# Kernel optimization log

Hardware: AMD Instinct MI355X
Metric: run time of the kernel (lower is better)

## Reference

```python
import jax, jax.numpy as jnp
import numpy as np

N_NODES = 50000
N_EDGES = 800000
IN_F = 128
HID = 256
N_CLS = 10
NUM_GRAPHS = 256


def setup_inputs() -> dict:
    key = jax.random.key(0)
    ks = jax.random.split(key, 8)
    x = jax.random.normal(ks[0], (N_NODES, IN_F), dtype=jnp.float32)
    edge_index = jax.random.randint(ks[1], (2, N_EDGES), 0, N_NODES, dtype=jnp.int64)
    batch = jnp.sort(jax.random.randint(ks[2], (N_NODES,), 0, NUM_GRAPHS, dtype=jnp.int64))
    # Glorot-style init for weights (GCNConv default), zeros bias
    W1 = jax.random.normal(ks[3], (IN_F, HID), dtype=jnp.float32) / np.sqrt(IN_F)
    b1 = jnp.zeros((HID,), dtype=jnp.float32)
    W2 = jax.random.normal(ks[4], (HID, HID), dtype=jnp.float32) / np.sqrt(HID)
    b2 = jnp.zeros((HID,), dtype=jnp.float32)
    Wlin = jax.random.normal(ks[5], (HID, N_CLS), dtype=jnp.float32) / np.sqrt(HID)
    blin = jnp.zeros((N_CLS,), dtype=jnp.float32)
    return {"x": x, "edge_index": edge_index, "batch": batch,
            "W1": W1, "b1": b1, "W2": W2, "b2": b2, "Wlin": Wlin, "blin": blin}


def reference(x, edge_index, batch, W1, b1, W2, b2, Wlin, blin):
    N = x.shape[0]
    # PyG GCNConv default: add self-loops, symmetric normalization D^-1/2 A D^-1/2
    loop = jnp.arange(N, dtype=edge_index.dtype)
    src = jnp.concatenate([edge_index[0], loop])  # message source (row)
    dst = jnp.concatenate([edge_index[1], loop])  # aggregation target (col)
    deg = jax.ops.segment_sum(jnp.ones_like(dst, dtype=x.dtype), dst, num_segments=N)
    dinv = jnp.where(deg > 0, jax.lax.rsqrt(deg), 0.0)
    norm = dinv[src] * dinv[dst]  # [E+N]

    def gcn_conv(h, W, b):
        h = h @ W                          # linear transform first (GCNConv)
        msg = h[src] * norm[:, None]       # gather + edge scale
        agg = jax.ops.segment_sum(msg, dst, num_segments=N)  # scatter-add
        return agg + b

    h = jax.nn.relu(gcn_conv(x, W1, b1))
    h = gcn_conv(h, W2, b2)

    # global_mean_pool over batch ids
    counts = jax.ops.segment_sum(jnp.ones((N,), x.dtype), batch, num_segments=NUM_GRAPHS)
    pooled = jax.ops.segment_sum(h, batch, num_segments=NUM_GRAPHS)
    pooled = pooled / jnp.maximum(counts, 1.0)[:, None]  # [NUM_GRAPHS, HID]

    return pooled @ Wlin + blin  # forward returns logits (softmax unused in forward)
```

## Files before the change

kernel.cpp:

```cpp
#include <hip/hip_runtime.h>
#include <hip/hip_bf16.h>

typedef __hip_bfloat16 bf16;
typedef __attribute__((ext_vector_type(8))) short short8;
typedef __attribute__((ext_vector_type(4))) float f32x4;
typedef __attribute__((ext_vector_type(2))) float f32x2;

#define N_NODES 50000
#define N_EDGES 800000
#define IN_F    128
#define HID     256
#define N_CLS   10
#define N_GRAPH 256

#define NB 98
#define PBLOCKS 256

__device__ __forceinline__ int IG(const int* __restrict__ p, int i, int w) {
    return w ? p[2 * i] : p[i];
}
__device__ __forceinline__ float LF(const void* __restrict__ p, int i, int isbf) {
    return isbf ? __bfloat162float(((const bf16*)p)[i]) : ((const float*)p)[i];
}
__device__ __forceinline__ float b2f(unsigned short h) {
    union { unsigned u; float f; } c; c.u = ((unsigned)h) << 16; return c.f;
}
__device__ __forceinline__ unsigned short f2b(float x) {
    bf16 h = __float2bfloat16(x);
    union { bf16 b; unsigned short u; } c; c.b = h; return c.u;
}
__device__ __forceinline__ float f8s(unsigned b) {
    union { unsigned u; float f; } c;
    c.u = ((b & 0x80u) << 24) | ((b & 0x7Fu) << 20);
    return c.f;
}
#define F8SCALE 0x1p120f
__device__ __forceinline__ unsigned f2fp8(float x) {
    unsigned short h = f2b(x * 0x1p-120f);
    unsigned s = ((unsigned)h >> 8) & 0x80u;
    unsigned mag = (unsigned)h & 0x7FFFu;
    unsigned r = (mag + 7u + ((mag >> 4) & 1u)) >> 4;
    if (r > 0x7Eu) r = 0x7Eu;
    return s | r;
}

#if defined(__has_builtin)
#if __has_builtin(__builtin_amdgcn_cvt_pk_f32_fp8)
#define HW_FP8 1
#endif
#if __has_builtin(__builtin_amdgcn_cvt_pk_fp8_f32)
#define HW_FP8E 1
#endif
#endif

__device__ __forceinline__ f32x2 cvt2lo(unsigned v) {
#ifdef HW_FP8
    return __builtin_amdgcn_cvt_pk_f32_fp8((int)v, false);
#else
    f32x2 r; r[0] = f8s(v & 0xFF) * F8SCALE; r[1] = f8s((v >> 8) & 0xFF) * F8SCALE; return r;
#endif
}
__device__ __forceinline__ f32x2 cvt2hi(unsigned v) {
#ifdef HW_FP8
    return __builtin_amdgcn_cvt_pk_f32_fp8((int)v, true);
#else
    f32x2 r; r[0] = f8s((v >> 16) & 0xFF) * F8SCALE; r[1] = f8s(v >> 24) * F8SCALE; return r;
#endif
}
__device__ __forceinline__ unsigned pk4_fp8(float v0, float v1, float v2, float v3) {
#ifdef HW_FP8E
    int o = __builtin_amdgcn_cvt_pk_fp8_f32(v0, v1, 0, false);
    o = __builtin_amdgcn_cvt_pk_fp8_f32(v2, v3, o, true);
    return (unsigned)o;
#else
    return f2fp8(v0) | (f2fp8(v1) << 8) | (f2fp8(v2) << 16) | (f2fp8(v3) << 24);
#endif
}

__global__ __launch_bounds__(256) void k_detect(const int* __restrict__ ei,
                                                const unsigned short* __restrict__ x,
                                                int* __restrict__ flags) {
    __shared__ int nz, cnt;
    if (threadIdx.x == 0) { nz = 0; cnt = 0; }
    __syncthreads();
    int found = 0, c = 0;
    for (int s = 0; s < 4; ++s) {
        int idx = 2 * (threadIdx.x * 4 + s) + 1;
        if (ei[idx] != 0) found = 1;
    }
    for (int s = 0; s < 8; ++s) {
        unsigned short h = x[threadIdx.x * 8 + s];
        int e = (h >> 7) & 0xFF;
        if (e >= 110 && e <= 135) c++;
    }
    if (found) atomicAdd(&nz, 1);
    atomicAdd(&cnt, c);
    __syncthreads();
    if (threadIdx.x == 0) {
        flags[0] = (nz == 0) ? 1 : 0;
        flags[1] = (cnt > 1536) ? 1 : 0;
    }
}

__global__ __launch_bounds__(256) void k_partA1(const int* __restrict__ ei, int* __restrict__ bucketCnt,
                                                int* __restrict__ blockBase, const int* __restrict__ flags,
                                                int E, int N) {
    __shared__ int h[NB];
    int t = threadIdx.x;
    if (t < NB) h[t] = 0;
    __syncthreads();
    int w = flags[0];
    for (int e = blockIdx.x * 256 + t; e < E; e += PBLOCKS * 256) {
        int d = IG(ei, E + e, w);
        int s = IG(ei, e, w);
        if ((unsigned)d < (unsigned)N && (unsigned)s < (unsigned)N)
            atomicAdd(&h[d >> 9], 1);
    }
    __syncthreads();
    if (t < NB)
        blockBase[blockIdx.x * NB + t] = atomicAdd(&bucketCnt[t * 16], h[t]);
}

__global__ __launch_bounds__(128) void k_bscan(const int* __restrict__ bucketCnt,
                                               int* __restrict__ bucketBase) {
    __shared__ int s[128];
    int t = threadIdx.x;
    int v = (t < NB) ? bucketCnt[t * 16] : 0;
    s[t] = v;
    __syncthreads();
    for (int off = 1; off < 128; off <<= 1) {
        int add = (t >= off) ? s[t - off] : 0;
        __syncthreads();
        s[t] += add;
        __syncthreads();
    }
    if (t <= NB) bucketBase[t] = (t < NB) ? (s[t] - v) : s[NB - 1] + 0;
    if (t == NB - 1) bucketBase[NB] = s[t];
}

__global__ __launch_bounds__(256) void k_partA2(const int* __restrict__ ei,
                                                const int* __restrict__ bucketBase,
                                                const int* __restrict__ blockBase,
                                                unsigned* __restrict__ part,
                                                const int* __restrict__ flags, int E, int N) {
    __shared__ int cur[NB];
    int t = threadIdx.x;
    if (t < NB) cur[t] = bucketBase[t] + blockBase[blockIdx.x * NB + t];
    __syncthreads();
    int w = flags[0];
    for (int e = blockIdx.x * 256 + t; e < E; e += PBLOCKS * 256) {
        int d = IG(ei, E + e, w);
        int s = IG(ei, e, w);
        if ((unsigned)d < (unsigned)N && (unsigned)s < (unsigned)N) {
            int slot = atomicAdd(&cur[d >> 9], 1);
            part[slot] = ((unsigned)(d & 511) << 16) | (unsigned)s;
        }
    }
}

__global__ __launch_bounds__(256) void k_partB(const unsigned* __restrict__ part,
                                               const int* __restrict__ bucketBase,
                                               int* __restrict__ rowptr, float* __restrict__ dinv,
                                               int* __restrict__ col, int N) {
    __shared__ int hist[512];
    __shared__ int scn[512];
    __shared__ int pair[256];
    int b = blockIdx.x, t = threadIdx.x;
    int s0 = bucketBase[b], e0 = bucketBase[b + 1];
    hist[t] = 0; hist[t + 256] = 0;
    __syncthreads();
    for (int j = s0 + t; j < e0; j += 256)
        atomicAdd(&hist[part[j] >> 16], 1);
    __syncthreads();
    int a0 = hist[2 * t], a1 = hist[2 * t + 1];
    int pv = a0 + a1;
    pair[t] = pv;
    __syncthreads();
    for (int off = 1; off < 256; off <<= 1) {
        int add = (t >= off) ? pair[t - off] : 0;
        __syncthreads();
        pair[t] += add;
        __syncthreads();
    }
    int pbase = pair[t] - pv;
    scn[2 * t] = pbase;
    scn[2 * t + 1] = pbase + a0;
    __syncthreads();
#pragma unroll
    for (int hh = 0; hh < 2; ++hh) {
        int l = t + hh * 256;
        int node = b * 512 + l;
        if (node < N) {
            rowptr[node] = s0 + scn[l];
            dinv[node] = rsqrtf((float)(hist[l] + 1));
        }
    }
    if (b == 0 && t == 0) rowptr[N] = bucketBase[NB];
    __syncthreads();
    for (int j = s0 + t; j < e0; j += 256) {
        unsigned p = part[j];
        int pos = s0 + atomicAdd(&scn[p >> 16], 1);
        col[pos] = (int)(p & 0xFFFFu);
    }
}

#define CVTX_BLOCKS 6250
#define CVT1_BLOCKS 128
#define CVT2_BLOCKS 256
#define GB_BLOCKS   196
__global__ __launch_bounds__(256) void k_cvt(const void* __restrict__ x, const float* __restrict__ dinv,
                                             unsigned char* __restrict__ xs8,
                                             const void* __restrict__ W1, unsigned short* __restrict__ w1t,
                                             const void* __restrict__ W2, unsigned short* __restrict__ w2t,
                                             const int* __restrict__ batch, int* __restrict__ gstart,
                                             const int* __restrict__ flags) {
    int b = blockIdx.x;
    int fb = flags[1];
    if (b < CVTX_BLOCKS) {
        int gid = b * 256 + threadIdx.x;
        int row = gid >> 5;
        float d = dinv[row];
        float vx, vy, vz, vw;
        if (fb) {
            ushort4 v = ((const ushort4*)x)[gid];
            vx = b2f(v.x); vy = b2f(v.y); vz = b2f(v.z); vw = b2f(v.w);
        } else {
            float4 v = ((const float4*)x)[gid];
            vx = v.x; vy = v.y; vz = v.z; vw = v.w;
        }
        ((unsigned*)xs8)[gid] = pk4_fp8(vx * d, vy * d, vz * d, vw * d);
    } else if (b < CVTX_BLOCKS + CVT1_BLOCKS) {
        int i = (b - CVTX_BLOCKS) * 256 + threadIdx.x;
        int n = i >> 7, k = i & 127;
        w1t[i] = f2b(LF(W1, k * 256 + n, fb));
    } else if (b < CVTX_BLOCKS + CVT1_BLOCKS + CVT2_BLOCKS) {
        int i = (b - CVTX_BLOCKS - CVT1_BLOCKS) * 256 + threadIdx.x;
        int n = i >> 8, k = i & 255;
        w2t[i] = f2b(LF(W2, k * 256 + n, fb));
    } else {
        int i = (b - CVTX_BLOCKS - CVT1_BLOCKS - CVT2_BLOCKS) * 256 + threadIdx.x;
        if (i <= N_NODES) {
            int w = flags[0];
            int prev = (i == 0) ? -1 : IG(batch, i - 1, w);
            int cur  = (i == N_NODES) ? N_GRAPH : IG(batch, i, w);
            if (prev < -1) prev = -1;
            if (cur > N_GRAPH) cur = N_GRAPH;
            for (int g = prev + 1; g <= cur; ++g)
                if (g >= 0 && g <= N_GRAPH) gstart[g] = i;
        }
    }
}

#define BSTR 132
__global__ __launch_bounds__(256) void k_gemm(const unsigned short* __restrict__ A,
                                              const unsigned short* __restrict__ Bt,
                                              unsigned short* __restrict__ C,
                                              unsigned char* __restrict__ C8, int M, int K,
                                              const float* __restrict__ rowscale,
                                              const void* __restrict__ bias,
                                              const int* __restrict__ flags, int relu) {
    __shared__ unsigned short Bs[128 * BSTR];
    int t = threadIdx.x;
    int lane = t & 63;
    int w = t >> 6;
    int stripe = blockIdx.y;
    int bm = blockIdx.x * 128;
    int l15 = lane & 15, quad = lane >> 4;
    const short8 Z8 = {0, 0, 0, 0, 0, 0, 0, 0};
    f32x4 acc[2][8];
#pragma unroll
    for (int i = 0; i < 2; ++i)
#pragma unroll
        for (int j = 0; j < 8; ++j) acc[i][j] = (f32x4){0.f, 0.f, 0.f, 0.f};

    int row0 = bm + w * 32 + l15;
    int row1 = row0 + 16;
    for (int kp = 0; kp < K; kp += 128) {
        if (kp) __syncthreads();
        {
            int n = t >> 1, h = t & 1;
            const unsigned short* src = &Bt[(size_t)(stripe * 128 + n) * K + kp + h * 64];
            unsigned short* dst = &Bs[n * BSTR + h * 64];
#pragma unroll
            for (int j = 0; j < 8; ++j)
                *(uint4*)&dst[j * 8] = *(const uint4*)&src[j * 8];
        }
        __syncthreads();
#pragma unroll
        for (int ks = 0; ks < 4; ++ks) {
            const unsigned short* abase = &A[(size_t)row0 * K + kp + ks * 32 + quad * 8];
            short8 a0 = (row0 < M) ? *(const short8*)abase : Z8;
            short8 a1 = (row1 < M) ? *(const short8*)(abase + (size_t)16 * K) : Z8;
#pragma unroll
            for (int tt = 0; tt < 8; ++tt) {
                short8 b = *(const short8*)&Bs[(tt * 16 + l15) * BSTR + ks * 32 + quad * 8];
                acc[0][tt] = __builtin_amdgcn_mfma_f32_16x16x32_bf16(b, a0, acc[0][tt], 0, 0, 0);
                acc[1][tt] = __builtin_amdgcn_mfma_f32_16x16x32_bf16(b, a1, acc[1][tt], 0, 0, 0);
            }
        }
    }
    int fb = flags[1];
    int rowA[2];
    float drow[2];
#pragma unroll
    for (int sa = 0; sa < 2; ++sa) {
        rowA[sa] = bm + w * 32 + sa * 16 + l15;
        drow[sa] = (rowscale && rowA[sa] < M) ? rowscale[rowA[sa]] : 1.f;
    }
    __syncthreads();
    if (C8) {
        unsigned* Cs = (unsigned*)Bs;
#pragma unroll
        for (int tt = 0; tt < 8; ++tt) {
            int colb = stripe * 128 + tt * 16 + quad * 4;
            float bc[4];
#pragma unroll
            for (int rr = 0; rr < 4; ++rr)
                bc[rr] = bias ? LF(bias, colb + rr, fb) : 0.f;
#pragma unroll
            for (int sa = 0; sa < 2; ++sa) {
                float v[4];
#pragma unroll
                for (int rr = 0; rr < 4; ++rr) {
                    float u = fmaf(acc[sa][tt][rr], drow[sa], bc[rr]);
                    v[rr] = relu ? fmaxf(u, 0.f) : u;
                }
                Cs[(w * 32 + sa * 16 + l15) * 36 + tt * 4 + quad] =
                    pk4_fp8(v[0], v[1], v[2], v[3]);
            }
        }
        __syncthreads();
        int r = t >> 1, h = t & 1;
        int grow = bm + r;
        if (grow < M) {
            const uint4* src = (const uint4*)(Cs + r * 36 + h * 16);
            uint4* dst = (uint4*)&C8[(size_t)grow * 256 + stripe * 128 + h * 64];
#pragma unroll
            for (int j = 0; j < 4; ++j) dst[j] = src[j];
        }
    } else {
        unsigned short* Cs = Bs;
#pragma unroll
        for (int tt = 0; tt < 8; ++tt) {
            int colb = stripe * 128 + tt * 16 + quad * 4;
            float bc[4];
#pragma unroll
            for (int rr = 0; rr < 4; ++rr)
                bc[rr] = bias ? LF(bias, colb + rr, fb) : 0.f;
#pragma unroll
            for (int sa = 0; sa < 2; ++sa) {
                float v[4];
#pragma unroll
                for (int rr = 0; rr < 4; ++rr) {
                    float u = fmaf(acc[sa][tt][rr], drow[sa], bc[rr]);
                    v[rr] = relu ? fmaxf(u, 0.f) : u;
                }
                ushort4 o;
                o.x = f2b(v[0]); o.y = f2b(v[1]); o.z = f2b(v[2]); o.w = f2b(v[3]);
                *(ushort4*)&Cs[(w * 32 + sa * 16 + l15) * 132 + tt * 16 + quad * 4] = o;
            }
        }
        __syncthreads();
        int r = t >> 1, h = t & 1;
        int grow = bm + r;
        if (grow < M) {
            int base = r * 132 + h * 64;
            size_t gbase = (size_t)grow * 256 + stripe * 128 + h * 64;
#pragma unroll
            for (int j = 0; j < 8; ++j) {
                uint2 a2 = *(const uint2*)&Cs[base + j * 8];
                uint2 b2 = *(const uint2*)&Cs[base + j * 8 + 4];
                uint4 u; u.x = a2.x; u.y = a2.y; u.z = b2.x; u.w = b2.y;
                *(uint4*)&C[gbase + j * 8] = u;
            }
        }
    }
}

__global__ __launch_bounds__(256) void k_agg2(const unsigned char* __restrict__ XS,
                                              const int* __restrict__ rowptr, const int* __restrict__ col,
                                              unsigned short* __restrict__ Hout, int N) {
    int lane = threadIdx.x & 63;
    int i = (blockIdx.x * 256 + threadIdx.x) >> 6;
    if (i >= N) return;
    int fo = lane * 2;
    unsigned sv = *(const unsigned short*)&XS[(size_t)i * 128 + fo];
    f32x2 a = cvt2lo(sv);
    int s = rowptr[i], e = rowptr[i + 1];
    int j = s;
    while (j + 16 <= e) {
        unsigned v[16];
#pragma unroll
        for (int q = 0; q < 16; ++q)
            v[q] = *(const unsigned short*)&XS[(size_t)col[j + q] * 128 + fo];
#pragma unroll
        for (int q = 0; q < 16; ++q) a += cvt2lo(v[q]);
        j += 16;
    }
    if (j + 8 <= e) {
        unsigned v[8];
#pragma unroll
        for (int q = 0; q < 8; ++q)
            v[q] = *(const unsigned short*)&XS[(size_t)col[j + q] * 128 + fo];
#pragma unroll
        for (int q = 0; q < 8; ++q) a += cvt2lo(v[q]);
        j += 8;
    }
    if (j + 4 <= e) {
        unsigned v[4];
#pragma unroll
        for (int q = 0; q < 4; ++q)
            v[q] = *(const unsigned short*)&XS[(size_t)col[j + q] * 128 + fo];
#pragma unroll
        for (int q = 0; q < 4; ++q) a += cvt2lo(v[q]);
        j += 4;
    }
    for (; j < e; ++j)
        a += cvt2lo(*(const unsigned short*)&XS[(size_t)col[j] * 128 + fo]);
    ushort2 o;
    o.x = f2b(a[0]); o.y = f2b(a[1]);
    *(ushort2*)&Hout[(size_t)i * 128 + fo] = o;
}

__global__ __launch_bounds__(256) void k_agg4(const unsigned char* __restrict__ XW,
                                              const int* __restrict__ rowptr, const int* __restrict__ col,
                                              const float* __restrict__ dinv, const void* __restrict__ bias,
                                              const int* __restrict__ flags,
                                              unsigned short* __restrict__ Hout, int N) {
    int lane = threadIdx.x & 63;
    int i = (blockIdx.x * 256 + threadIdx.x) >> 6;
    if (i >= N) return;
    int fo = lane * 4;
    unsigned sv = *(const unsigned*)&XW[(size_t)i * 256 + fo];
    f32x2 a01 = cvt2lo(sv), a23 = cvt2hi(sv);
    int s = rowptr[i], e = rowptr[i + 1];
    int j = s;
    while (j + 16 <= e) {
        unsigned v[16];
#pragma unroll
        for (int q = 0; q < 16; ++q)
            v[q] = *(const unsigned*)&XW[(size_t)col[j + q] * 256 + fo];
#pragma unroll
        for (int q = 0; q < 16; ++q) { a01 += cvt2lo(v[q]); a23 += cvt2hi(v[q]); }
        j += 16;
    }
    if (j + 8 <= e) {
        unsigned v[8];
#pragma unroll
        for (int q = 0; q < 8; ++q)
            v[q] = *(const unsigned*)&XW[(size_t)col[j + q] * 256 + fo];
#pragma unroll
        for (int q = 0; q < 8; ++q) { a01 += cvt2lo(v[q]); a23 += cvt2hi(v[q]); }
        j += 8;
    }
    if (j + 4 <= e) {
        unsigned v[4];
#pragma unroll
        for (int q = 0; q < 4; ++q)
            v[q] = *(const unsigned*)&XW[(size_t)col[j + q] * 256 + fo];
#pragma unroll
        for (int q = 0; q < 4; ++q) { a01 += cvt2lo(v[q]); a23 += cvt2hi(v[q]); }
        j += 4;
    }
    for (; j < e; ++j) {
        unsigned v = *(const unsigned*)&XW[(size_t)col[j] * 256 + fo];
        a01 += cvt2lo(v); a23 += cvt2hi(v);
    }
    int fb = flags[1];
    float di = dinv[i];
    float bx = LF(bias, fo + 0, fb), by = LF(bias, fo + 1, fb);
    float bz = LF(bias, fo + 2, fb), bw = LF(bias, fo + 3, fb);
    ushort4 o;
    o.x = f2b(fmaf(a01[0], di, bx)); o.y = f2b(fmaf(a01[1], di, by));
    o.z = f2b(fmaf(a23[0], di, bz)); o.w = f2b(fmaf(a23[1], di, bw));
    *(ushort4*)&Hout[(size_t)i * 256 + fo] = o;
}

__global__ __launch_bounds__(256) void k_poolfinal(const unsigned short* __restrict__ H2,
                                                   const int* __restrict__ gstart,
                                                   const void* __restrict__ Wlin,
                                                   const void* __restrict__ blin,
                                                   const int* __restrict__ flags,
                                                   void* __restrict__ outv) {
    __shared__ float red[4][256];
    __shared__ float p[256];
    int g = blockIdx.x, t = threadIdx.x;
    int sub = t >> 6, lane = t & 63;
    int s = gstart[g], e = gstart[g + 1];
    int cnt = e - s;
    float ax = 0.f, ay = 0.f, az = 0.f, aw = 0.f;
    for (int i = s + sub; i < e; i += 4) {
        ushort4 v = *(const ushort4*)&H2[(size_t)i * 256 + lane * 4];
        ax += b2f(v.x); ay += b2f(v.y); az += b2f(v.z); aw += b2f(v.w);
    }
    red[sub][lane * 4 + 0] = ax;
    red[sub][lane * 4 + 1] = ay;
    red[sub][lane * 4 + 2] = az;
    red[sub][lane * 4 + 3] = aw;
    __syncthreads();
    float inv = 1.f / fmaxf((float)cnt, 1.f);
    p[t] = (red[0][t] + red[1][t] + red[2][t] + red[3][t]) * inv;
    __syncthreads();
    int fb = flags[1];
    if (t < N_CLS) {
        float sum = LF(blin, t, fb);
        for (int f = 0; f < HID; ++f) sum = fmaf(p[f], LF(Wlin, f * N_CLS + t, fb), sum);
        if (fb) ((bf16*)outv)[g * N_CLS + t] = __float2bfloat16(sum);
        else    ((float*)outv)[g * N_CLS + t] = sum;
    }
}

extern "C" void kernel_launch(void* const* d_in, const int* in_sizes, int n_in,
                              void* d_out, int out_size, void* d_ws, size_t ws_size,
                              hipStream_t stream) {
    (void)n_in; (void)ws_size; (void)in_sizes; (void)out_size;
    const void* x     = d_in[0];
    const int*  ei    = (const int*)d_in[1];
    const int*  batch = (const int*)d_in[2];
    const void* W1    = d_in[3];
    const void* b1    = d_in[4];
    const void* W2    = d_in[5];
    const void* b2    = d_in[6];
    const void* Wl    = d_in[7];
    const void* bl    = d_in[8];

    const int N = N_NODES, E = N_EDGES, F = IN_F, H = HID, G = N_GRAPH;

    char* ws = (char*)d_ws;
    size_t off = 0;
    auto alloc = [&](size_t bytes) -> void* {
        void* p = ws + off;
        off += (bytes + 511) & ~(size_t)511;
        return p;
    };
    unsigned char*  xs8  = (unsigned char*)alloc((size_t)N * F);
    unsigned short* aggX = (unsigned short*)alloc((size_t)N * F * 2);
    unsigned short* H1   = (unsigned short*)alloc((size_t)N * H * 2);
    unsigned short* H2   = (unsigned short*)alloc((size_t)N * H * 2);
    unsigned char*  XW2s8 = xs8;
    unsigned short* w1t  = (unsigned short*)alloc((size_t)H * F * 2);
    unsigned short* w2t  = (unsigned short*)alloc((size_t)H * H * 2);
    int*   bucketCnt = (int*)alloc((size_t)NB * 16 * 4);
    int*   bucketBase = (int*)alloc((size_t)(NB + 1) * 4);
    int*   blockBase = (int*)alloc((size_t)PBLOCKS * NB * 4);
    unsigned* part  = (unsigned*)alloc((size_t)E * 4);
    int*   gstart  = (int*)alloc((size_t)(G + 1) * 4);
    float* dinv    = (float*)alloc((size_t)N * 4);
    int*   rowptr  = (int*)alloc((size_t)(N + 1) * 4);
    int*   flags   = (int*)alloc(512);
    int*   col     = (int*)alloc((size_t)E * 4);
    size_t zero_bytes = (size_t)NB * 16 * 4;

    hipMemsetAsync(bucketCnt, 0, zero_bytes, stream);

    k_detect<<<1, 256, 0, stream>>>(ei, (const unsigned short*)x, flags);
    k_partA1<<<PBLOCKS, 256, 0, stream>>>(ei, bucketCnt, blockBase, flags, E, N);
    k_bscan<<<1, 128, 0, stream>>>(bucketCnt, bucketBase);
    k_partA2<<<PBLOCKS, 256, 0, stream>>>(ei, bucketBase, blockBase, part, flags, E, N);
    k_partB<<<NB, 256, 0, stream>>>(part, bucketBase, rowptr, dinv, col, N);

    k_cvt<<<CVTX_BLOCKS + CVT1_BLOCKS + CVT2_BLOCKS + GB_BLOCKS, 256, 0, stream>>>(
        x, dinv, xs8, W1, w1t, W2, w2t, batch, gstart, flags);

    dim3 gemmGrid((N + 127) / 128, 2);
    int nbAgg = (N + 3) / 4;

    k_agg2<<<nbAgg, 256, 0, stream>>>(xs8, rowptr, col, aggX, N);
    k_gemm<<<gemmGrid, 256, 0, stream>>>(aggX, w1t, H1, nullptr, N, F, dinv, b1, flags, 1);
    k_gemm<<<gemmGrid, 256, 0, stream>>>(H1, w2t, nullptr, XW2s8, N, H, dinv, nullptr, flags, 0);
    k_agg4<<<nbAgg, 256, 0, stream>>>(XW2s8, rowptr, col, dinv, b2, flags, H2, N);
    k_poolfinal<<<G, 256, 0, stream>>>(H2, gstart, Wl, bl, flags, d_out);
}
```

Baseline: 282.8 us.

## Restructure GEMM to full-width 64-row tiles with register-prefetched direct global operands

The GEMM kernel no longer stages the B (weight) stripe in shared memory. Each block now covers 64 rows and all 256 output columns, and each wave owns a 64-column slice. A and B fragments are loaded straight from global memory into registers, with a one-step software prefetch of the next K slice. This removes the shared-memory staging and barriers and the second column-stripe grid dimension, so each A row is read once instead of twice. The cost is higher register pressure and B fragments reloaded from global/L2 by every block, with no LDS reuse.

```diff
diff --git a/kernel.cpp b/kernel.cpp
--- a/kernel.cpp
+++ b/kernel.cpp
@@ -251,7 +251,6 @@
     }
 }
 
-#define BSTR 132
 __global__ __launch_bounds__(256) void k_gemm(const unsigned short* __restrict__ A,
                                               const unsigned short* __restrict__ Bt,
                                               unsigned short* __restrict__ C,
@@ -259,120 +258,122 @@
                                               const float* __restrict__ rowscale,
                                               const void* __restrict__ bias,
                                               const int* __restrict__ flags, int relu) {
-    __shared__ unsigned short Bs[128 * BSTR];
+    __shared__ unsigned char lds[64 * 132 * 4];
     int t = threadIdx.x;
     int lane = t & 63;
     int w = t >> 6;
-    int stripe = blockIdx.y;
-    int bm = blockIdx.x * 128;
+    int bm = blockIdx.x * 64;
     int l15 = lane & 15, quad = lane >> 4;
-    const short8 Z8 = {0, 0, 0, 0, 0, 0, 0, 0};
-    f32x4 acc[2][8];
-#pragma unroll
-    for (int i = 0; i < 2; ++i)
-#pragma unroll
-        for (int j = 0; j < 8; ++j) acc[i][j] = (f32x4){0.f, 0.f, 0.f, 0.f};
-
-    int row0 = bm + w * 32 + l15;
-    int row1 = row0 + 16;
-    for (int kp = 0; kp < K; kp += 128) {
-        if (kp) __syncthreads();
-        {
-            int n = t >> 1, h = t & 1;
-            const unsigned short* src = &Bt[(size_t)(stripe * 128 + n) * K + kp + h * 64];
-            unsigned short* dst = &Bs[n * BSTR + h * 64];
-#pragma unroll
-            for (int j = 0; j < 8; ++j)
-                *(uint4*)&dst[j * 8] = *(const uint4*)&src[j * 8];
-        }
-        __syncthreads();
-#pragma unroll
-        for (int ks = 0; ks < 4; ++ks) {
-            const unsigned short* abase = &A[(size_t)row0 * K + kp + ks * 32 + quad * 8];
-            short8 a0 = (row0 < M) ? *(const short8*)abase : Z8;
-            short8 a1 = (row1 < M) ? *(const short8*)(abase + (size_t)16 * K) : Z8;
-#pragma unroll
-            for (int tt = 0; tt < 8; ++tt) {
-                short8 b = *(const short8*)&Bs[(tt * 16 + l15) * BSTR + ks * 32 + quad * 8];
-                acc[0][tt] = __builtin_amdgcn_mfma_f32_16x16x32_bf16(b, a0, acc[0][tt], 0, 0, 0);
-                acc[1][tt] = __builtin_amdgcn_mfma_f32_16x16x32_bf16(b, a1, acc[1][tt], 0, 0, 0);
-            }
-        }
-    }
+
+    f32x4 acc[4][4];
+#pragma unroll
+    for (int ar = 0; ar < 4; ++ar)
+#pragma unroll
+        for (int tt = 0; tt < 4; ++tt) acc[ar][tt] = (f32x4){0.f, 0.f, 0.f, 0.f};
+
+    const unsigned short* ap[4];
+    const unsigned short* bp[4];
+#pragma unroll
+    for (int ar = 0; ar < 4; ++ar)
+        ap[ar] = &A[(size_t)(bm + ar * 16 + l15) * K + quad * 8];
+#pragma unroll
+    for (int tt = 0; tt < 4; ++tt)
+        bp[tt] = &Bt[(size_t)(w * 64 + tt * 16 + l15) * K + quad * 8];
+
+    int nks = K >> 5;
+    short8 a[4], b[4];
+#pragma unroll
+    for (int ar = 0; ar < 4; ++ar) a[ar] = *(const short8*)(ap[ar]);
+#pragma unroll
+    for (int tt = 0; tt < 4; ++tt) b[tt] = *(const short8*)(bp[tt]);
+    for (int ks = 0; ks < nks; ++ks) {
+        short8 an[4], bn[4];
+        int nxt = (ks + 1) * 32;
+        if (ks + 1 < nks) {
+#pragma unroll
+            for (int ar = 0; ar < 4; ++ar) an[ar] = *(const short8*)(ap[ar] + nxt);
+#pragma unroll
+            for (int tt = 0; tt < 4; ++tt) bn[tt] = *(const short8*)(bp[tt] + nxt);
+        }
+#pragma unroll
+        for (int ar = 0; ar < 4; ++ar)
+#pragma unroll
+            for (int tt = 0; tt < 4; ++tt)
+                acc[ar][tt] = __builtin_amdgcn_mfma_f32_16x16x32_bf16(b[tt], a[ar], acc[ar][tt], 0, 0, 0);
+        if (ks + 1 < nks) {
+#pragma unroll
+            for (int ar = 0; ar < 4; ++ar) a[ar] = an[ar];
+#pragma unroll
+            for (int tt = 0; tt < 4; ++tt) b[tt] = bn[tt];
+        }
+    }
+
     int fb = flags[1];
-    int rowA[2];
-    float drow[2];
-#pragma unroll
-    for (int sa = 0; sa < 2; ++sa) {
-        rowA[sa] = bm + w * 32 + sa * 16 + l15;
-        drow[sa] = (rowscale && rowA[sa] < M) ? rowscale[rowA[sa]] : 1.f;
-    }
-    __syncthreads();
+    float drow[4];
+#pragma unroll
+    for (int ar = 0; ar < 4; ++ar) {
+        int row = bm + ar * 16 + l15;
+        drow[ar] = (rowscale && row < M) ? rowscale[row] : 1.f;
+    }
     if (C8) {
-        unsigned* Cs = (unsigned*)Bs;
-#pragma unroll
-        for (int tt = 0; tt < 8; ++tt) {
-            int colb = stripe * 128 + tt * 16 + quad * 4;
+        unsigned* Cs = (unsigned*)lds;
+#pragma unroll
+        for (int tt = 0; tt < 4; ++tt) {
+            int colb = w * 64 + tt * 16 + quad * 4;
             float bc[4];
 #pragma unroll
             for (int rr = 0; rr < 4; ++rr)
                 bc[rr] = bias ? LF(bias, colb + rr, fb) : 0.f;
 #pragma unroll
-            for (int sa = 0; sa < 2; ++sa) {
+            for (int ar = 0; ar < 4; ++ar) {
                 float v[4];
 #pragma unroll
                 for (int rr = 0; rr < 4; ++rr) {
-                    float u = fmaf(acc[sa][tt][rr], drow[sa], bc[rr]);
+                    float u = fmaf(acc[ar][tt][rr], drow[ar], bc[rr]);
                     v[rr] = relu ? fmaxf(u, 0.f) : u;
                 }
-                Cs[(w * 32 + sa * 16 + l15) * 36 + tt * 4 + quad] =
+                Cs[(ar * 16 + l15) * 68 + w * 16 + tt * 4 + quad] =
                     pk4_fp8(v[0], v[1], v[2], v[3]);
             }
         }
         __syncthreads();
-        int r = t >> 1, h = t & 1;
-        int grow = bm + r;
-        if (grow < M) {
-            const uint4* src = (const uint4*)(Cs + r * 36 + h * 16);
-            uint4* dst = (uint4*)&C8[(size_t)grow * 256 + stripe * 128 + h * 64];
-#pragma unroll
-            for (int j = 0; j < 4; ++j) dst[j] = src[j];
+        int r = t >> 2, h = t & 3;
+        if (bm + r < M) {
+            const unsigned* src = Cs + r * 68 + h * 16;
+            uint4* dst = (uint4*)&C8[(size_t)(bm + r) * 256 + h * 64];
+#pragma unroll
+            for (int j = 0; j < 4; ++j) dst[j] = *(const uint4*)(src + j * 4);
         }
     } else {
-        unsigned short* Cs = Bs;
-#pragma unroll
-        for (int tt = 0; tt < 8; ++tt) {
-            int colb = stripe * 128 + tt * 16 + quad * 4;
+        unsigned short* Cs = (unsigned short*)lds;
+#pragma unroll
+        for (int tt = 0; tt < 4; ++tt) {
+            int colb = w * 64 + tt * 16 + quad * 4;
             float bc[4];
 #pragma unroll
             for (int rr = 0; rr < 4; ++rr)
                 bc[rr] = bias ? LF(bias, colb + rr, fb) : 0.f;
 #pragma unroll
-            for (int sa = 0; sa < 2; ++sa) {
+            for (int ar = 0; ar < 4; ++ar) {
                 float v[4];
 #pragma unroll
                 for (int rr = 0; rr < 4; ++rr) {
-                    float u = fmaf(acc[sa][tt][rr], drow[sa], bc[rr]);
+                    float u = fmaf(acc[ar][tt][rr], drow[ar], bc[rr]);
                     v[rr] = relu ? fmaxf(u, 0.f) : u;
                 }
                 ushort4 o;
                 o.x = f2b(v[0]); o.y = f2b(v[1]); o.z = f2b(v[2]); o.w = f2b(v[3]);
-                *(ushort4*)&Cs[(w * 32 + sa * 16 + l15) * 132 + tt * 16 + quad * 4] = o;
+                *(ushort4*)&Cs[(ar * 16 + l15) * 264 + w * 64 + tt * 16 + quad * 4] = o;
             }
         }
         __syncthreads();
-        int r = t >> 1, h = t & 1;
-        int grow = bm + r;
-        if (grow < M) {
-            int base = r * 132 + h * 64;
-            size_t gbase = (size_t)grow * 256 + stripe * 128 + h * 64;
-#pragma unroll
-            for (int j = 0; j < 8; ++j) {
-                uint2 a2 = *(const uint2*)&Cs[base + j * 8];
-                uint2 b2 = *(const uint2*)&Cs[base + j * 8 + 4];
-                uint4 u; u.x = a2.x; u.y = a2.y; u.z = b2.x; u.w = b2.y;
-                *(uint4*)&C[gbase + j * 8] = u;
-            }
+        int r = t >> 2, h = t & 3;
+        if (bm + r < M) {
+            int base = r * 264 + h * 64;
+            size_t g = (size_t)(bm + r) * 256 + h * 64;
+#pragma unroll
+            for (int j = 0; j < 8; ++j)
+                *(uint4*)&C[g + j * 8] = *(const uint4*)&Cs[base + j * 8];
         }
     }
 }
@@ -562,12 +563,12 @@
     k_cvt<<<CVTX_BLOCKS + CVT1_BLOCKS + CVT2_BLOCKS + GB_BLOCKS, 256, 0, stream>>>(
         x, dinv, xs8, W1, w1t, W2, w2t, batch, gstart, flags);
 
-    dim3 gemmGrid((N + 127) / 128, 2);
+    int gemmBlocks = (N + 63) / 64;
     int nbAgg = (N + 3) / 4;
 
     k_agg2<<<nbAgg, 256, 0, stream>>>(xs8, rowptr, col, aggX, N);
-    k_gemm<<<gemmGrid, 256, 0, stream>>>(aggX, w1t, H1, nullptr, N, F, dinv, b1, flags, 1);
-    k_gemm<<<gemmGrid, 256, 0, stream>>>(H1, w2t, nullptr, XW2s8, N, H, dinv, nullptr, flags, 0);
+    k_gemm<<<gemmBlocks, 256, 0, stream>>>(aggX, w1t, H1, nullptr, N, F, dinv, b1, flags, 1);
+    k_gemm<<<gemmBlocks, 256, 0, stream>>>(H1, w2t, nullptr, XW2s8, N, H, dinv, nullptr, flags, 0);
     k_agg4<<<nbAgg, 256, 0, stream>>>(XW2s8, rowptr, col, dinv, b2, flags, H2, N);
     k_poolfinal<<<G, 256, 0, stream>>>(H2, gstart, Wl, bl, flags, d_out);
 }
```

New measurement: 289.8 us. 2.5% more time.

## Fuse second aggregation with mean pooling and remap GEMM/agg block order

Applied to the files above, without the earlier changes.

The second-layer aggregation now accumulates normalized node features straight into a per-graph fp32 pooled buffer with atomics, using a shared-memory reduction when all four nodes in a block share a graph. This removes the H2 write and re-read. The bias is applied once per graph in the final kernel. The GEMM and first aggregation grids are remapped into groups of eight row tiles so neighbouring blocks cover nearby rows and both output stripes of a tile run close together, which is meant to improve L2 reuse. Atomics add contention and make the result order nondeterministic, and an extra memset is needed.

```diff
diff --git a/kernel.cpp b/kernel.cpp
--- a/kernel.cpp
+++ b/kernel.cpp
@@ -263,15 +263,18 @@
     int t = threadIdx.x;
     int lane = t & 63;
     int w = t >> 6;
-    int stripe = blockIdx.y;
-    int bm = blockIdx.x * 128;
+    int i = blockIdx.x;
+    int grp = i >> 4, stripe = (i >> 3) & 1, x8 = i & 7;
+    int bx = grp * 8 + x8;
+    int bm = bx * 128;
+    if (bm >= M) return;
     int l15 = lane & 15, quad = lane >> 4;
     const short8 Z8 = {0, 0, 0, 0, 0, 0, 0, 0};
     f32x4 acc[2][8];
 #pragma unroll
-    for (int i = 0; i < 2; ++i)
-#pragma unroll
-        for (int j = 0; j < 8; ++j) acc[i][j] = (f32x4){0.f, 0.f, 0.f, 0.f};
+    for (int ii = 0; ii < 2; ++ii)
+#pragma unroll
+        for (int j = 0; j < 8; ++j) acc[ii][j] = (f32x4){0.f, 0.f, 0.f, 0.f};
 
     int row0 = bm + w * 32 + l15;
     int row1 = row0 + 16;
@@ -380,8 +383,12 @@
 __global__ __launch_bounds__(256) void k_agg2(const unsigned char* __restrict__ XS,
                                               const int* __restrict__ rowptr, const int* __restrict__ col,
                                               unsigned short* __restrict__ Hout, int N) {
+    int jb = blockIdx.x;
+    int x8 = jb & 7, k = jb >> 3;
+    int gIdx = k >> 5, win = k & 31;
+    int node0 = (gIdx * 8 + x8) * 128 + win * 4;
     int lane = threadIdx.x & 63;
-    int i = (blockIdx.x * 256 + threadIdx.x) >> 6;
+    int i = node0 + (threadIdx.x >> 6);
     if (i >= N) return;
     int fo = lane * 2;
     unsigned sv = *(const unsigned short*)&XS[(size_t)i * 128 + fo];
@@ -422,86 +429,100 @@
     *(ushort2*)&Hout[(size_t)i * 128 + fo] = o;
 }
 
-__global__ __launch_bounds__(256) void k_agg4(const unsigned char* __restrict__ XW,
-                                              const int* __restrict__ rowptr, const int* __restrict__ col,
-                                              const float* __restrict__ dinv, const void* __restrict__ bias,
-                                              const int* __restrict__ flags,
-                                              unsigned short* __restrict__ Hout, int N) {
-    int lane = threadIdx.x & 63;
-    int i = (blockIdx.x * 256 + threadIdx.x) >> 6;
-    if (i >= N) return;
+__global__ __launch_bounds__(256) void k_agg4pool(const unsigned char* __restrict__ XW,
+                                                  const int* __restrict__ rowptr, const int* __restrict__ col,
+                                                  const float* __restrict__ dinv,
+                                                  const int* __restrict__ batch,
+                                                  const int* __restrict__ flags,
+                                                  float* __restrict__ pooled, int N) {
+    __shared__ float red[4][256];
+    __shared__ int gs[4];
+    int t = threadIdx.x;
+    int lane = t & 63, sub = t >> 6;
+    int i = blockIdx.x * 4 + sub;
     int fo = lane * 4;
-    unsigned sv = *(const unsigned*)&XW[(size_t)i * 256 + fo];
-    f32x2 a01 = cvt2lo(sv), a23 = cvt2hi(sv);
-    int s = rowptr[i], e = rowptr[i + 1];
-    int j = s;
-    while (j + 16 <= e) {
-        unsigned v[16];
-#pragma unroll
-        for (int q = 0; q < 16; ++q)
-            v[q] = *(const unsigned*)&XW[(size_t)col[j + q] * 256 + fo];
-#pragma unroll
-        for (int q = 0; q < 16; ++q) { a01 += cvt2lo(v[q]); a23 += cvt2hi(v[q]); }
-        j += 16;
-    }
-    if (j + 8 <= e) {
-        unsigned v[8];
-#pragma unroll
-        for (int q = 0; q < 8; ++q)
-            v[q] = *(const unsigned*)&XW[(size_t)col[j + q] * 256 + fo];
-#pragma unroll
-        for (int q = 0; q < 8; ++q) { a01 += cvt2lo(v[q]); a23 += cvt2hi(v[q]); }
-        j += 8;
-    }
-    if (j + 4 <= e) {
-        unsigned v[4];
-#pragma unroll
-        for (int q = 0; q < 4; ++q)
-            v[q] = *(const unsigned*)&XW[(size_t)col[j + q] * 256 + fo];
-#pragma unroll
-        for (int q = 0; q < 4; ++q) { a01 += cvt2lo(v[q]); a23 += cvt2hi(v[q]); }
-        j += 4;
-    }
-    for (; j < e; ++j) {
-        unsigned v = *(const unsigned*)&XW[(size_t)col[j] * 256 + fo];
-        a01 += cvt2lo(v); a23 += cvt2hi(v);
-    }
-    int fb = flags[1];
-    float di = dinv[i];
-    float bx = LF(bias, fo + 0, fb), by = LF(bias, fo + 1, fb);
-    float bz = LF(bias, fo + 2, fb), bw = LF(bias, fo + 3, fb);
-    ushort4 o;
-    o.x = f2b(fmaf(a01[0], di, bx)); o.y = f2b(fmaf(a01[1], di, by));
-    o.z = f2b(fmaf(a23[0], di, bz)); o.w = f2b(fmaf(a23[1], di, bw));
-    *(ushort4*)&Hout[(size_t)i * 256 + fo] = o;
-}
-
-__global__ __launch_bounds__(256) void k_poolfinal(const unsigned short* __restrict__ H2,
+    float v[4] = {0.f, 0.f, 0.f, 0.f};
+    int g = -1;
+    if (i < N) {
+        g = IG(batch, i, flags[0]);
+        unsigned sv = *(const unsigned*)&XW[(size_t)i * 256 + fo];
+        f32x2 a01 = cvt2lo(sv), a23 = cvt2hi(sv);
+        int s = rowptr[i], e = rowptr[i + 1];
+        int j = s;
+        while (j + 16 <= e) {
+            unsigned vv[16];
+#pragma unroll
+            for (int q = 0; q < 16; ++q)
+                vv[q] = *(const unsigned*)&XW[(size_t)col[j + q] * 256 + fo];
+#pragma unroll
+            for (int q = 0; q < 16; ++q) { a01 += cvt2lo(vv[q]); a23 += cvt2hi(vv[q]); }
+            j += 16;
+        }
+        if (j + 8 <= e) {
+            unsigned vv[8];
+#pragma unroll
+            for (int q = 0; q < 8; ++q)
+                vv[q] = *(const unsigned*)&XW[(size_t)col[j + q] * 256 + fo];
+#pragma unroll
+            for (int q = 0; q < 8; ++q) { a01 += cvt2lo(vv[q]); a23 += cvt2hi(vv[q]); }
+            j += 8;
+        }
+        if (j + 4 <= e) {
+            unsigned vv[4];
+#pragma unroll
+            for (int q = 0; q < 4; ++q)
+                vv[q] = *(const unsigned*)&XW[(size_t)col[j + q] * 256 + fo];
+#pragma unroll
+            for (int q = 0; q < 4; ++q) { a01 += cvt2lo(vv[q]); a23 += cvt2hi(vv[q]); }
+            j += 4;
+        }
+        for (; j < e; ++j) {
+            unsigned vv = *(const unsigned*)&XW[(size_t)col[j] * 256 + fo];
+            a01 += cvt2lo(vv); a23 += cvt2hi(vv);
+        }
+        float di = dinv[i];
+        v[0] = a01[0] * di; v[1] = a01[1] * di;
+        v[2] = a23[0] * di; v[3] = a23[1] * di;
+    }
+    if (lane == 0) gs[sub] = g;
+#pragma unroll
+    for (int k2 = 0; k2 < 4; ++k2) red[sub][fo + k2] = v[k2];
+    __syncthreads();
+    int g0 = gs[0];
+    bool uni = (gs[1] == g0 || gs[1] < 0) && (gs[2] == g0 || gs[2] < 0) &&
+               (gs[3] == g0 || gs[3] < 0);
+    if (uni) {
+        if (sub == 0 && g0 >= 0) {
+#pragma unroll
+            for (int k2 = 0; k2 < 4; ++k2) {
+                float sv2 = red[0][fo + k2] + red[1][fo + k2] +
+                            red[2][fo + k2] + red[3][fo + k2];
+                atomicAdd(&pooled[g0 * 256 + fo + k2], sv2);
+            }
+        }
+    } else if (g >= 0) {
+#pragma unroll
+        for (int k2 = 0; k2 < 4; ++k2)
+            atomicAdd(&pooled[g * 256 + fo + k2], v[k2]);
+    }
+}
+
+__global__ __launch_bounds__(256) void k_poolfinal(const float* __restrict__ pooled,
                                                    const int* __restrict__ gstart,
+                                                   const void* __restrict__ b2,
                                                    const void* __restrict__ Wlin,
                                                    const void* __restrict__ blin,
                                                    const int* __restrict__ flags,
                                                    void* __restrict__ outv) {
-    __shared__ float red[4][256];
     __shared__ float p[256];
     int g = blockIdx.x, t = threadIdx.x;
-    int sub = t >> 6, lane = t & 63;
     int s = gstart[g], e = gstart[g + 1];
     int cnt = e - s;
-    float ax = 0.f, ay = 0.f, az = 0.f, aw = 0.f;
-    for (int i = s + sub; i < e; i += 4) {
-        ushort4 v = *(const ushort4*)&H2[(size_t)i * 256 + lane * 4];
-        ax += b2f(v.x); ay += b2f(v.y); az += b2f(v.z); aw += b2f(v.w);
-    }
-    red[sub][lane * 4 + 0] = ax;
-    red[sub][lane * 4 + 1] = ay;
-    red[sub][lane * 4 + 2] = az;
-    red[sub][lane * 4 + 3] = aw;
-    __syncthreads();
+    int fb = flags[1];
     float inv = 1.f / fmaxf((float)cnt, 1.f);
-    p[t] = (red[0][t] + red[1][t] + red[2][t] + red[3][t]) * inv;
-    __syncthreads();
-    int fb = flags[1];
+    float bb = (cnt > 0) ? LF(b2, t, fb) : 0.f;
+    p[t] = pooled[g * 256 + t] * inv + bb;
+    __syncthreads();
     if (t < N_CLS) {
         float sum = LF(blin, t, fb);
         for (int f = 0; f < HID; ++f) sum = fmaf(p[f], LF(Wlin, f * N_CLS + t, fb), sum);
@@ -536,7 +557,7 @@
     unsigned char*  xs8  = (unsigned char*)alloc((size_t)N * F);
     unsigned short* aggX = (unsigned short*)alloc((size_t)N * F * 2);
     unsigned short* H1   = (unsigned short*)alloc((size_t)N * H * 2);
-    unsigned short* H2   = (unsigned short*)alloc((size_t)N * H * 2);
+    float*          pooled = (float*)alloc((size_t)G * H * 4);
     unsigned char*  XW2s8 = xs8;
     unsigned short* w1t  = (unsigned short*)alloc((size_t)H * F * 2);
     unsigned short* w2t  = (unsigned short*)alloc((size_t)H * H * 2);
@@ -552,6 +573,7 @@
     size_t zero_bytes = (size_t)NB * 16 * 4;
 
     hipMemsetAsync(bucketCnt, 0, zero_bytes, stream);
+    hipMemsetAsync(pooled, 0, (size_t)G * H * 4, stream);
 
     k_detect<<<1, 256, 0, stream>>>(ei, (const unsigned short*)x, flags);
     k_partA1<<<PBLOCKS, 256, 0, stream>>>(ei, bucketCnt, blockBase, flags, E, N);
@@ -560,14 +582,16 @@
     k_partB<<<NB, 256, 0, stream>>>(part, bucketBase, rowptr, dinv, col, N);
 
     k_cvt<<<CVTX_BLOCKS + CVT1_BLOCKS + CVT2_BLOCKS + GB_BLOCKS, 256, 0, stream>>>(
-        x, dinv, xs8, W1, w1t, W2, w2t, batch, gstart, flags);
-
-    dim3 gemmGrid((N + 127) / 128, 2);
-    int nbAgg = (N + 3) / 4;
-
-    k_agg2<<<nbAgg, 256, 0, stream>>>(xs8, rowptr, col, aggX, N);
-    k_gemm<<<gemmGrid, 256, 0, stream>>>(aggX, w1t, H1, nullptr, N, F, dinv, b1, flags, 1);
-    k_gemm<<<gemmGrid, 256, 0, stream>>>(H1, w2t, nullptr, XW2s8, N, H, dinv, nullptr, flags, 0);
-    k_agg4<<<nbAgg, 256, 0, stream>>>(XW2s8, rowptr, col, dinv, b2, flags, H2, N);
-    k_poolfinal<<<G, 256, 0, stream>>>(H2, gstart, Wl, bl, flags, d_out);
-}
+        x, dinv, xs8, W1, w1t, w2t ? W2 : W2, w2t, batch, gstart, flags);
+
+    int mB = (N + 127) >> 7;
+    int gemmBlocks = ((mB + 7) >> 3) * 16;
+    int aggBlocks = ((mB + 7) >> 3) * 8 * 32;
+    int poolBlocks = (N + 3) / 4;
+
+    k_agg2<<<aggBlocks, 256, 0, stream>>>(xs8, rowptr, col, aggX, N);
+    k_gemm<<<gemmBlocks, 256, 0, stream>>>(aggX, w1t, H1, nullptr, N, F, dinv, b1, flags, 1);
+    k_gemm<<<gemmBlocks, 256, 0, stream>>>(H1, w2t, nullptr, XW2s8, N, H, dinv, nullptr, flags, 0);
+    k_agg4pool<<<poolBlocks, 256, 0, stream>>>(XW2s8, rowptr, col, dinv, batch, flags, pooled, N);
+    k_poolfinal<<<G, 256, 0, stream>>>(pooled, gstart, b2, Wl, bl, flags, d_out);
+}
```

After: 302.0 us. 6.8% more time.
